# Kernel optimization log

Hardware: AMD Instinct MI355X
Metric: run time of the kernel (lower is better)

The kernel has to match this reference:

```python
import jax, jax.numpy as jnp
import numpy as np

LAYER_SIZES = [3, 3, 3]
CHANNELS = 192
BATCH = 65536
FULL_SIZES = [1] + LAYER_SIZES + [1]  # 1 -> 3 -> 3 -> 3 -> 1
NUM_LAYERS = len(LAYER_SIZES) + 1     # 4


def setup_inputs() -> dict:
    key = jax.random.key(0)
    ks = jax.random.split(key, 1 + len(LAYER_SIZES) + NUM_LAYERS + NUM_LAYERS)
    inp = {"x": jax.random.normal(ks[0], (BATCH, CHANNELS, 1), dtype=jnp.float32)}
    i = 1
    for k, sz in enumerate(LAYER_SIZES):
        inp[f"a{k}"] = jax.random.normal(ks[i], (CHANNELS, sz), dtype=jnp.float32); i += 1
    for k in range(NUM_LAYERS):  # b[k] has size full_sizes[k+1]
        inp[f"b{k}"] = jax.random.normal(ks[i], (CHANNELS, FULL_SIZES[k + 1]), dtype=jnp.float32); i += 1
    for k in range(NUM_LAYERS):
        inp[f"H{k}"] = jax.random.normal(ks[i], (CHANNELS, FULL_SIZES[k], FULL_SIZES[k + 1]), dtype=jnp.float32); i += 1
    return inp


def _cdf(x, a_list, b_list, H_list):
    # x: (B, C, 1)
    for k in range(NUM_LAYERS - 1):
        # per-channel matmul: (B,C,M) x (C,M,P) -> (B,C,P), with softplus-constrained H
        x = jnp.einsum('bni,nip->bnp', x, jax.nn.softplus(H_list[k])) + b_list[k]
        x = x + jnp.tanh(a_list[k]) * jnp.tanh(x)
    x = jnp.einsum('bni,nip->bnp', x, jax.nn.softplus(H_list[-1])) + b_list[-1]
    return jax.nn.sigmoid(x)


def reference(x, a0, a1, a2, b0, b1, b2, b3, H0, H1, H2, H3):
    a_list = [a0, a1, a2]
    b_list = [b0, b1, b2, b3]
    H_list = [H0, H1, H2, H3]
    # PDF of y_tilde: c(x + 1/2) - c(x - 1/2)
    half = jnp.asarray(0.5, dtype=x.dtype)
    p = _cdf(x + half, a_list, b_list, H_list) - _cdf(x - half, a_list, b_list, H_list)
    return p
```

## Files before the change

### kernel.cpp

```cpp
#include <hip/hip_runtime.h>
#include <hip/hip_bf16.h>
#include <math.h>

#define CHN 192
#define BATCHN 65536
#define NBLOCKS 4096
#define ROWS_PER_BLOCK (BATCHN / NBLOCKS)
#define NWS 61

#define KSCALE 2.885390081777926f
#define LOG2E  1.4426950408889634f

__device__ __forceinline__ float fast_rcp(float x)  { return __builtin_amdgcn_rcpf(x); }
__device__ __forceinline__ float fast_exp2(float x) { return __builtin_amdgcn_exp2f(x); }
__device__ __forceinline__ void pinf(float& v) { asm volatile("" : "+v"(v)); }

__device__ __forceinline__ float softplus_acc(float h) {
    if (h > 20.0f) return h;
    return log1pf(expf(h));
}

__global__ __launch_bounds__(CHN) void weights_kernel(
    const float* __restrict__ a0, const float* __restrict__ a1, const float* __restrict__ a2,
    const float* __restrict__ b0, const float* __restrict__ b1, const float* __restrict__ b2,
    const float* __restrict__ b3,
    const float* __restrict__ H0, const float* __restrict__ H1, const float* __restrict__ H2,
    const float* __restrict__ H3,
    float* __restrict__ ws)
{
    const int c = threadIdx.x;
#pragma unroll
    for (int i = 0; i < 3; ++i) {
        float w0k = KSCALE * softplus_acc(H0[c * 3 + i]);
        float h   = 0.5f * w0k;
        float t1k0 = KSCALE * tanhf(a0[c * 3 + i]);
        ws[(0  + i) * CHN + c] = w0k;
        ws[(3  + i) * CHN + c] = KSCALE * b0[c * 3 + i];
        ws[(6  + i) * CHN + c] = exp2f(h);
        ws[(9  + i) * CHN + c] = exp2f(-h);
        ws[(12 + i) * CHN + c] = h + t1k0;
        ws[(15 + i) * CHN + c] = -h + t1k0;
        ws[(18 + i) * CHN + c] = -2.0f * t1k0;

        float t1k1 = KSCALE * tanhf(a1[c * 3 + i]);
        ws[(30 + i) * CHN + c] = KSCALE * b1[c * 3 + i];
        ws[(33 + i) * CHN + c] = t1k1;
        ws[(36 + i) * CHN + c] = -2.0f * t1k1;

        float t1k2 = KSCALE * tanhf(a2[c * 3 + i]);
        ws[(48 + i) * CHN + c] = KSCALE * b2[c * 3 + i];
        ws[(51 + i) * CHN + c] = t1k2;
        ws[(54 + i) * CHN + c] = -2.0f * t1k2;

        ws[(57 + i) * CHN + c] = -0.5f * softplus_acc(H3[c * 3 + i]);
    }
#pragma unroll
    for (int i = 0; i < 9; ++i) {
        ws[(21 + i) * CHN + c] = softplus_acc(H1[c * 9 + i]);
        ws[(39 + i) * CHN + c] = softplus_acc(H2[c * 9 + i]);
    }
    ws[60 * CHN + c] = -LOG2E * b3[c];
}

__device__ __forceinline__ float density_pair(const float* __restrict__ W, float xv) {
    float vp[3], vm[3];
#pragma unroll
    for (int i = 0; i < 3; ++i) {
        float q  = fmaf(W[0 + i], xv, W[3 + i]);
        float E  = fast_exp2(q);
        float rp = fast_rcp(fmaf(E, W[6 + i], 1.0f));
        float rm = fast_rcp(fmaf(E, W[9 + i], 1.0f));
        vp[i] = fmaf(W[18 + i], rp, q + W[12 + i]);
        vm[i] = fmaf(W[18 + i], rm, q + W[15 + i]);
    }
    float zp[3], zm[3];
#pragma unroll
    for (int p = 0; p < 3; ++p) {
        float tp = W[30 + p], tm = W[30 + p];
#pragma unroll
        for (int i = 0; i < 3; ++i) {
            tp = fmaf(vp[i], W[21 + i * 3 + p], tp);
            tm = fmaf(vm[i], W[21 + i * 3 + p], tm);
        }
        float rp = fast_rcp(fast_exp2(tp) + 1.0f);
        float rm = fast_rcp(fast_exp2(tm) + 1.0f);
        zp[p] = fmaf(W[36 + p], rp, tp + W[33 + p]);
        zm[p] = fmaf(W[36 + p], rm, tm + W[33 + p]);
    }
    float yp[3], ym[3];
#pragma unroll
    for (int p = 0; p < 3; ++p) {
        float tp = W[48 + p], tm = W[48 + p];
#pragma unroll
        for (int i = 0; i < 3; ++i) {
            tp = fmaf(zp[i], W[39 + i * 3 + p], tp);
            tm = fmaf(zm[i], W[39 + i * 3 + p], tm);
        }
        float rp = fast_rcp(fast_exp2(tp) + 1.0f);
        float rm = fast_rcp(fast_exp2(tm) + 1.0f);
        yp[p] = fmaf(W[54 + p], rp, tp + W[51 + p]);
        ym[p] = fmaf(W[54 + p], rm, tm + W[51 + p]);
    }
    float sp = W[60], sm = W[60];
#pragma unroll
    for (int i = 0; i < 3; ++i) {
        sp = fmaf(yp[i], W[57 + i], sp);
        sm = fmaf(ym[i], W[57 + i], sm);
    }
    float pp = fast_rcp(fast_exp2(sp) + 1.0f);
    float pm = fast_rcp(fast_exp2(sm) + 1.0f);
    return pp - pm;
}

__global__ __launch_bounds__(CHN) void density_kernel(
    const float* __restrict__ x,
    const float* __restrict__ wt,
    float* __restrict__ out)
{
    const int c = threadIdx.x;

    float W[NWS];
#pragma unroll
    for (int s = 0; s < NWS; ++s) W[s] = wt[s * CHN + c];
#pragma unroll
    for (int s = 0; s < NWS; ++s) pinf(W[s]);

    const int b_start = blockIdx.x * ROWS_PER_BLOCK;
#pragma unroll 2
    for (int r = 0; r < ROWS_PER_BLOCK; ++r) {
        const int idx = (b_start + r) * CHN + c;
        out[idx] = density_pair(W, x[idx]);
    }
}

extern "C" void kernel_launch(void* const* d_in, const int* in_sizes, int n_in,
                              void* d_out, int out_size, void* d_ws, size_t ws_size,
                              hipStream_t stream) {
    const float* x  = (const float*)d_in[0];
    const float* a0 = (const float*)d_in[1];
    const float* a1 = (const float*)d_in[2];
    const float* a2 = (const float*)d_in[3];
    const float* b0 = (const float*)d_in[4];
    const float* b1 = (const float*)d_in[5];
    const float* b2 = (const float*)d_in[6];
    const float* b3 = (const float*)d_in[7];
    const float* H0 = (const float*)d_in[8];
    const float* H1 = (const float*)d_in[9];
    const float* H2 = (const float*)d_in[10];
    const float* H3 = (const float*)d_in[11];
    float* out = (float*)d_out;
    float* ws  = (float*)d_ws;

    weights_kernel<<<1, CHN, 0, stream>>>(a0, a1, a2, b0, b1, b2, b3,
                                          H0, H1, H2, H3, ws);
    density_kernel<<<NBLOCKS, CHN, 0, stream>>>(x, ws, out);
}
```

Baseline: 81.76 us.

## Make channel weights wave-uniform scalars via LDS tile transpose

Restructures the density kernel so each wave processes one channel across 64 batch rows, with the per-channel weights read with readfirstlane so they can live in scalar registers instead of 61 VGPRs. The x tile is staged through padded LDS using float4 global loads and stores, then transposed so each lane handles a different row. This is meant to cut vector register pressure and raise occupancy, and to keep wide coalesced global accesses. In exchange it adds LDS traffic, two block barriers, and a reload of the weights for every channel iteration.

```diff
diff --git a/kernel.cpp b/kernel.cpp
--- a/kernel.cpp
+++ b/kernel.cpp
@@ -4,16 +4,23 @@
 
 #define CHN 192
 #define BATCHN 65536
-#define NBLOCKS 4096
-#define ROWS_PER_BLOCK (BATCHN / NBLOCKS)
-#define NWS 61
+#define NS  61
+#define WSTRIDE 64
+#define TROWS 64
+#define PAD 193
+#define BLOCKT 768
+#define NWAVES (BLOCKT / 64)
+#define NITER (CHN / NWAVES)
+#define NTILES (BATCHN / TROWS)
 
 #define KSCALE 2.885390081777926f
 #define LOG2E  1.4426950408889634f
 
 __device__ __forceinline__ float fast_rcp(float x)  { return __builtin_amdgcn_rcpf(x); }
 __device__ __forceinline__ float fast_exp2(float x) { return __builtin_amdgcn_exp2f(x); }
-__device__ __forceinline__ void pinf(float& v) { asm volatile("" : "+v"(v)); }
+__device__ __forceinline__ float rfl(float v) {
+    return __int_as_float(__builtin_amdgcn_readfirstlane(__float_as_int(v)));
+}
 
 __device__ __forceinline__ float softplus_acc(float h) {
     if (h > 20.0f) return h;
@@ -29,37 +36,38 @@
     float* __restrict__ ws)
 {
     const int c = threadIdx.x;
+    float* wc = ws + c * WSTRIDE;
 #pragma unroll
     for (int i = 0; i < 3; ++i) {
-        float w0k = KSCALE * softplus_acc(H0[c * 3 + i]);
-        float h   = 0.5f * w0k;
+        float w0k  = KSCALE * softplus_acc(H0[c * 3 + i]);
+        float h    = 0.5f * w0k;
         float t1k0 = KSCALE * tanhf(a0[c * 3 + i]);
-        ws[(0  + i) * CHN + c] = w0k;
-        ws[(3  + i) * CHN + c] = KSCALE * b0[c * 3 + i];
-        ws[(6  + i) * CHN + c] = exp2f(h);
-        ws[(9  + i) * CHN + c] = exp2f(-h);
-        ws[(12 + i) * CHN + c] = h + t1k0;
-        ws[(15 + i) * CHN + c] = -h + t1k0;
-        ws[(18 + i) * CHN + c] = -2.0f * t1k0;
+        wc[0  + i] = w0k;
+        wc[3  + i] = KSCALE * b0[c * 3 + i];
+        wc[6  + i] = exp2f(h);
+        wc[9  + i] = exp2f(-h);
+        wc[12 + i] = h + t1k0;
+        wc[15 + i] = -h + t1k0;
+        wc[18 + i] = -2.0f * t1k0;
 
         float t1k1 = KSCALE * tanhf(a1[c * 3 + i]);
-        ws[(30 + i) * CHN + c] = KSCALE * b1[c * 3 + i];
-        ws[(33 + i) * CHN + c] = t1k1;
-        ws[(36 + i) * CHN + c] = -2.0f * t1k1;
+        wc[30 + i] = KSCALE * b1[c * 3 + i];
+        wc[33 + i] = t1k1;
+        wc[36 + i] = -2.0f * t1k1;
 
         float t1k2 = KSCALE * tanhf(a2[c * 3 + i]);
-        ws[(48 + i) * CHN + c] = KSCALE * b2[c * 3 + i];
-        ws[(51 + i) * CHN + c] = t1k2;
-        ws[(54 + i) * CHN + c] = -2.0f * t1k2;
+        wc[48 + i] = KSCALE * b2[c * 3 + i];
+        wc[51 + i] = t1k2;
+        wc[54 + i] = -2.0f * t1k2;
 
-        ws[(57 + i) * CHN + c] = -0.5f * softplus_acc(H3[c * 3 + i]);
+        wc[57 + i] = -0.5f * softplus_acc(H3[c * 3 + i]);
     }
 #pragma unroll
     for (int i = 0; i < 9; ++i) {
-        ws[(21 + i) * CHN + c] = softplus_acc(H1[c * 9 + i]);
-        ws[(39 + i) * CHN + c] = softplus_acc(H2[c * 9 + i]);
+        wc[21 + i] = softplus_acc(H1[c * 9 + i]);
+        wc[39 + i] = softplus_acc(H2[c * 9 + i]);
     }
-    ws[60 * CHN + c] = -LOG2E * b3[c];
+    wc[60] = -LOG2E * b3[c];
 }
 
 __device__ __forceinline__ float density_pair(const float* __restrict__ W, float xv) {
@@ -112,24 +120,51 @@
     return pp - pm;
 }
 
-__global__ __launch_bounds__(CHN) void density_kernel(
+__global__ __launch_bounds__(BLOCKT) void density_kernel(
     const float* __restrict__ x,
     const float* __restrict__ wt,
     float* __restrict__ out)
 {
-    const int c = threadIdx.x;
+    __shared__ float tile[TROWS * PAD];
 
-    float W[NWS];
+    const int tid  = threadIdx.x;
+    const int g0   = blockIdx.x * (TROWS * CHN);
+
+    const float4* x4 = reinterpret_cast<const float4*>(x + g0);
 #pragma unroll
-    for (int s = 0; s < NWS; ++s) W[s] = wt[s * CHN + c];
+    for (int v = 0; v < 4; ++v) {
+        int j = v * BLOCKT + tid;
+        float4 d = x4[j];
+        int li = 4 * j + j / 48;
+        tile[li + 0] = d.x; tile[li + 1] = d.y;
+        tile[li + 2] = d.z; tile[li + 3] = d.w;
+    }
+    __syncthreads();
+
+    const int w = __builtin_amdgcn_readfirstlane(tid >> 6);
+    const int l = tid & 63;
+    for (int k = 0; k < NITER; ++k) {
+        const int c = k * NWAVES + w;
+        const float* wc = wt + c * WSTRIDE;
+        float W[NS];
 #pragma unroll
-    for (int s = 0; s < NWS; ++s) pinf(W[s]);
+        for (int s = 0; s < NS; ++s) W[s] = rfl(wc[s]);
 
-    const int b_start = blockIdx.x * ROWS_PER_BLOCK;
-#pragma unroll 2
-    for (int r = 0; r < ROWS_PER_BLOCK; ++r) {
-        const int idx = (b_start + r) * CHN + c;
-        out[idx] = density_pair(W, x[idx]);
+        const int li = l * PAD + c;
+        float xv = tile[li];
+        tile[li] = density_pair(W, xv);
+    }
+    __syncthreads();
+
+    float4* o4 = reinterpret_cast<float4*>(out + g0);
+#pragma unroll
+    for (int v = 0; v < 4; ++v) {
+        int j = v * BLOCKT + tid;
+        int li = 4 * j + j / 48;
+        float4 d;
+        d.x = tile[li + 0]; d.y = tile[li + 1];
+        d.z = tile[li + 2]; d.w = tile[li + 3];
+        o4[j] = d;
     }
 }
 
@@ -153,5 +188,5 @@
 
     weights_kernel<<<1, CHN, 0, stream>>>(a0, a1, a2, b0, b1, b2, b3,
                                           H0, H1, H2, H3, ws);
-    density_kernel<<<NBLOCKS, CHN, 0, stream>>>(x, ws, out);
+    density_kernel<<<NTILES, BLOCKT, 0, stream>>>(x, ws, out);
 }
```

Measured after the change: 89.98 us. +10.0%, slower.
